# Kernel optimization log

Measured on AMD Instinct MI355X. Metric: run time of the kernel, lower is better.

Reference implementation:

```python
import jax, jax.numpy as jnp
import numpy as np

B, S, D = 2, 2048, 2048
H, KV, HD = 32, 8, 64          # n_heads, n_kv_heads, head_dim
REP = H // KV                  # 4
THETA = 10000.0


def _rotate_half(u):
    h = u.shape[-1] // 2
    return jnp.concatenate([-u[..., h:], u[..., :h]], axis=-1)


def setup_inputs() -> dict:
    key = jax.random.key(0)
    ks = jax.random.split(key, 5)
    x = jax.random.normal(ks[0], (B, S, D), dtype=jnp.float32)
    Wq = jax.random.normal(ks[1], (D, H * HD), dtype=jnp.float32) * 0.02
    Wk = jax.random.normal(ks[2], (D, KV * HD), dtype=jnp.float32) * 0.02
    Wv = jax.random.normal(ks[3], (D, KV * HD), dtype=jnp.float32) * 0.02
    Wo = jax.random.normal(ks[4], (H * HD, D), dtype=jnp.float32) * 0.02
    return {"x": x, "Wq": Wq, "Wk": Wk, "Wv": Wv, "Wo": Wo}


def reference(x, Wq, Wk, Wv, Wo):
    b, s, d = x.shape
    # QKV projections (nn.Linear, no bias)
    q = (x @ Wq).reshape(b, s, H, HD).transpose(0, 2, 1, 3)   # [B,H,S,HD]
    k = (x @ Wk).reshape(b, s, KV, HD).transpose(0, 2, 1, 3)  # [B,KV,S,HD]
    v = (x @ Wv).reshape(b, s, KV, HD).transpose(0, 2, 1, 3)  # [B,KV,S,HD]

    # RoPE (position_offset = 0)
    inv_freq = 1.0 / (THETA ** (jnp.arange(0, HD, 2, dtype=jnp.float32) / HD))
    freqs = jnp.outer(jnp.arange(s, dtype=jnp.float32), inv_freq)  # [S,HD/2]
    emb = jnp.concatenate([freqs, freqs], axis=-1)                  # [S,HD]
    cos, sin = jnp.cos(emb), jnp.sin(emb)
    q = q * cos + _rotate_half(q) * sin
    k = k * cos + _rotate_half(k) * sin

    # Grouped attention: avoid materializing repeated KV tensors.
    qg = q.reshape(b, KV, REP, s, HD)                               # [B,KV,REP,S,HD]
    scale = 1.0 / np.sqrt(HD)
    scores = jnp.einsum('bgrqd,bgkd->bgrqk', qg, k) * scale         # [B,KV,REP,S,S]
    causal = jnp.tril(jnp.ones((s, s), dtype=bool))
    scores = jnp.where(causal, scores, jnp.finfo(jnp.float32).min)
    probs = jax.nn.softmax(scores.astype(jnp.float32), axis=-1).astype(q.dtype)
    out = jnp.einsum('bgrqk,bgkd->bgrqd', probs, v)                 # [B,KV,REP,S,HD]
    out = out.reshape(b, H, s, HD).transpose(0, 2, 1, 3).reshape(b, s, H * HD)
    return out @ Wo                                                  # [B,S,D]
```

## Files before the change

kernel.cpp:

```cpp
#include <hip/hip_runtime.h>
#include <math.h>

typedef __bf16 bf16_t;
typedef bf16_t bf16x8 __attribute__((ext_vector_type(8)));
typedef bf16_t bf16x4 __attribute__((ext_vector_type(4)));
typedef float floatx4 __attribute__((ext_vector_type(4)));
typedef short short4v __attribute__((ext_vector_type(4)));

#define MFMA16(a, b, c) __builtin_amdgcn_mfma_f32_16x16x32_bf16((a), (b), (c), 0, 0, 0)

#if __has_builtin(__builtin_amdgcn_exp2f)
#define PEXP(x) __builtin_amdgcn_exp2f(x)
#define SCORE_SCALE (0.125f * 1.4426950408889634f)
#else
#define PEXP(x) __expf(x)
#define SCORE_SCALE 0.125f
#endif

#if __has_builtin(__builtin_amdgcn_mfma_f32_16x16x16bf16_1k)
#define HAVE_MFMA_K16 1
__device__ __forceinline__ floatx4 mfma_k16(bf16x4 a, bf16x4 b, floatx4 c)
{
    union { bf16x4 v; short4v s; } ua, ub;
    ua.v = a; ub.v = b;
    return __builtin_amdgcn_mfma_f32_16x16x16bf16_1k(ua.s, ub.s, c, 0, 0, 0);
}
#endif

union PU { unsigned u[2]; bf16x4 v; };
union BU { unsigned u[4]; bf16x8 v; };

__device__ __forceinline__ void gld16(const void* g, void* lds)
{
    __builtin_amdgcn_global_load_lds(
        reinterpret_cast<const __attribute__((address_space(1))) void*>(
            reinterpret_cast<uintptr_t>(g)),
        reinterpret_cast<__attribute__((address_space(3))) void*>(
            (unsigned int)reinterpret_cast<uintptr_t>(lds)),
        16, 0, 0);
}

template <int ROUNDS>
__device__ __forceinline__ void stage512(
    const bf16_t* __restrict__ g, int K, int row0, int k0,
    bf16_t* lds, int tid, int wave)
{
    #pragma unroll
    for (int i = 0; i < ROUNDS; ++i) {
        int c = i * 512 + tid;
        int r = c >> 3, s = c & 7;
        gld16(g + (size_t)(row0 + r) * K + k0 + ((s ^ (r & 7)) << 3),
              lds + (size_t)(i * 512 + wave * 64) * 8);
    }
}

template <typename TC, int BN>
__device__ __forceinline__ void gemm256_body(
    const bf16_t* __restrict__ A, const bf16_t* __restrict__ Bt,
    TC* __restrict__ C, int row0, int col0, int N, int K, bf16_t* smem)
{
    constexpr int NT = BN / 64;
    constexpr int RB = BN / 64;
    constexpr int LPT = 4 + RB;

    const int tid  = threadIdx.x;
    const int wave = tid >> 6, lane = tid & 63;
    const int quad = lane >> 4, l16 = lane & 15;
    const int wm = (wave >> 2) * 128;
    const int wn = (wave & 3) * (BN / 4);

    bf16_t* As0 = smem;
    bf16_t* As1 = smem + 256 * 64;
    bf16_t* Bs0 = smem + 2 * 256 * 64;
    bf16_t* Bs1 = Bs0 + BN * 64;

    floatx4 acc[8][NT] = {};

    const int ntile = K >> 6;

    stage512<4>(A, K, row0, 0, As0, tid, wave);
    stage512<RB>(Bt, K, col0, 0, Bs0, tid, wave);

    #pragma unroll 1
    for (int t = 0; t < ntile; ++t) {
        const int cur = t & 1;
        bf16_t* Asc = cur ? As1 : As0;
        bf16_t* Bsc = cur ? Bs1 : Bs0;
        bf16_t* Asn = cur ? As0 : As1;
        bf16_t* Bsn = cur ? Bs0 : Bs1;

        if (t + 1 < ntile) {
            stage512<4>(A, K, row0, (t + 1) << 6, Asn, tid, wave);
            stage512<RB>(Bt, K, col0, (t + 1) << 6, Bsn, tid, wave);
            if constexpr (LPT == 8)
                __asm__ volatile("s_waitcnt vmcnt(8)" ::: "memory");
            else
                __asm__ volatile("s_waitcnt vmcnt(6)" ::: "memory");
        } else {
            __asm__ volatile("s_waitcnt vmcnt(0)" ::: "memory");
        }
        __builtin_amdgcn_s_barrier();
        __asm__ volatile("" ::: "memory");

        #pragma unroll
        for (int kh = 0; kh < 2; ++kh) {
            bf16x8 af[8], bfr[NT];
            #pragma unroll
            for (int mt = 0; mt < 8; ++mt) {
                int ar = wm + mt * 16 + l16;
                af[mt] = *(const bf16x8*)&Asc[ar * 64 + (((kh * 4 + quad) ^ (ar & 7)) << 3)];
            }
            #pragma unroll
            for (int nt = 0; nt < NT; ++nt) {
                int br = wn + nt * 16 + l16;
                bfr[nt] = *(const bf16x8*)&Bsc[br * 64 + (((kh * 4 + quad) ^ (br & 7)) << 3)];
            }
            __builtin_amdgcn_s_setprio(1);
            #pragma unroll
            for (int mt = 0; mt < 8; ++mt)
                #pragma unroll
                for (int nt = 0; nt < NT; ++nt)
                    acc[mt][nt] = MFMA16(af[mt], bfr[nt], acc[mt][nt]);
            __builtin_amdgcn_s_setprio(0);
        }
        __asm__ volatile("s_waitcnt lgkmcnt(0)" ::: "memory");
        __builtin_amdgcn_s_barrier();
    }

    #pragma unroll
    for (int mt = 0; mt < 8; ++mt)
        #pragma unroll
        for (int nt = 0; nt < NT; ++nt)
            #pragma unroll
            for (int r = 0; r < 4; ++r)
                C[(size_t)(row0 + wm + mt * 16 + quad * 4 + r) * N
                  + col0 + wn + nt * 16 + l16] = (TC)acc[mt][nt][r];
}

__global__ __launch_bounds__(512, 2) void gemm256_qkv(
    const bf16_t* __restrict__ A, const bf16_t* __restrict__ BtQ,
    const bf16_t* __restrict__ BtK, const bf16_t* __restrict__ BtV,
    bf16_t* __restrict__ CQ, bf16_t* __restrict__ CK, bf16_t* __restrict__ CV)
{
    extern __shared__ __align__(16) bf16_t smem[];
    const int x = blockIdx.x;
    const bf16_t* Bt; bf16_t* C; int N, col0;
    if (x < 8)       { Bt = BtQ; C = CQ; N = 2048; col0 = x * 256; }
    else if (x < 10) { Bt = BtK; C = CK; N = 512;  col0 = (x - 8) * 256; }
    else             { Bt = BtV; C = CV; N = 512;  col0 = (x - 10) * 256; }
    gemm256_body<bf16_t, 256>(A, Bt, C, blockIdx.y * 256, col0, N, 2048, smem);
}

__global__ __launch_bounds__(512, 2) void gemm256_out(
    const bf16_t* __restrict__ A, const bf16_t* __restrict__ Bt,
    float* __restrict__ C)
{
    extern __shared__ __align__(16) bf16_t smem[];
    gemm256_body<float, 128>(A, Bt, C, blockIdx.y * 256, blockIdx.x * 128,
                             2048, 2048, smem);
}

__device__ __forceinline__ void transpose_body(
    const float* __restrict__ W, bf16_t* __restrict__ Wt, int K, int N,
    int bx, int by, float (*t)[33], int tid)
{
    int tx = tid & 31, ty = tid >> 5;
    #pragma unroll
    for (int i = 0; i < 32; i += 8)
        t[ty + i][tx] = W[(size_t)(by + ty + i) * N + bx + tx];
    __syncthreads();
    #pragma unroll
    for (int i = 0; i < 32; i += 8)
        Wt[(size_t)(bx + ty + i) * K + by + tx] = (bf16_t)t[tx][ty + i];
}

__global__ __launch_bounds__(256) void prep_all(
    const float* __restrict__ x, const float* __restrict__ Wq,
    const float* __restrict__ Wk, const float* __restrict__ Wv,
    bf16_t* __restrict__ xb, bf16_t* __restrict__ WqT,
    bf16_t* __restrict__ WkT, bf16_t* __restrict__ WvT)
{
    __shared__ float t[32][33];
    const int blk = blockIdx.x, tid = threadIdx.x;
    if (blk < 8192) {
        int i = blk * 256 + tid;
        float4 f = ((const float4*)x)[i];
        bf16x4 v = {(bf16_t)f.x, (bf16_t)f.y, (bf16_t)f.z, (bf16_t)f.w};
        ((bf16x4*)xb)[i] = v;
    } else if (blk < 12288) {
        int r = blk - 8192;
        transpose_body(Wq, WqT, 2048, 2048, (r & 63) * 32, (r >> 6) * 32, t, tid);
    } else if (blk < 13312) {
        int r = blk - 12288;
        transpose_body(Wk, WkT, 2048, 512, (r & 15) * 32, (r >> 4) * 32, t, tid);
    } else {
        int r = blk - 13312;
        transpose_body(Wv, WvT, 2048, 512, (r & 15) * 32, (r >> 4) * 32, t, tid);
    }
}

__global__ __launch_bounds__(256) void mid_all(
    bf16_t* __restrict__ Kw, const bf16_t* __restrict__ Vw,
    bf16_t* __restrict__ VtG, const float* __restrict__ Wo,
    bf16_t* __restrict__ WoT)
{
    __shared__ float tf[32][33];
    __shared__ bf16_t tb[32][34];
    const int blk = blockIdx.x, tid = threadIdx.x;
    if (blk < 4096) {
        int idx = blk * 256 + tid;
        int i   = idx & 31;
        int h   = (idx >> 5) & 7;
        int row = idx >> 8;
        int pos = row & 2047;
        float invf = powf(10000.0f, -(float)i / 32.0f);
        float sv, cv;
        sincosf((float)pos * invf, &sv, &cv);
        size_t base = (size_t)row * 512 + (size_t)h * 64 + i;
        float a  = (float)Kw[base];
        float b2 = (float)Kw[base + 32];
        Kw[base]      = (bf16_t)(a * cv - b2 * sv);
        Kw[base + 32] = (bf16_t)(b2 * cv + a * sv);
    } else if (blk < 6144) {
        int r  = blk - 4096;
        int bz = r >> 10, r2 = r & 1023;
        int bx = (r2 & 15) * 32, by = (r2 >> 4) * 32;
        int tx = tid & 31, ty = tid >> 5;
        #pragma unroll
        for (int i = 0; i < 32; i += 8)
            tb[ty + i][tx] = Vw[((size_t)bz * 2048 + by + ty + i) * 512 + bx + tx];
        __syncthreads();
        #pragma unroll
        for (int i = 0; i < 32; i += 8)
            VtG[((size_t)bz * 512 + bx + ty + i) * 2048 + by + tx] = tb[tx][ty + i];
    } else {
        int r = blk - 6144;
        transpose_body(Wo, WoT, 2048, 2048, (r & 63) * 32, (r >> 6) * 32, tf, tid);
    }
}

__global__ __launch_bounds__(256) void gqa_attn(
    const bf16_t* __restrict__ Q, const bf16_t* __restrict__ Kc,
    const bf16_t* __restrict__ Vt, bf16_t* __restrict__ AO)
{
    __shared__ alignas(16) bf16_t Ks[2][64 * 64];
    __shared__ alignas(16) bf16_t Vs[2][64 * 64];

    const int x = blockIdx.x, h = blockIdx.y, b = blockIdx.z, g = h >> 2;
    const int tid  = threadIdx.x;
    const int wave = tid >> 6, lane = tid & 63;
    const int quad = lane >> 4, l16 = lane & 15;

    #pragma unroll 1
    for (int t = 0; t < 2; ++t) {
        const int qt = t ? x : (15 - x);
        const int q0 = qt * 128;
        int qb[2];
        qb[0] = q0 + wave * 16;
        qb[1] = qb[0] + 64;

        bf16x8 qf[2][2];
        #pragma unroll
        for (int mt = 0; mt < 2; ++mt) {
            int qrow = qb[mt] + l16;
            const bf16_t* qp = Q + (size_t)(b * 2048 + qrow) * 2048 + h * 64 + quad * 8;
            bf16x8 lo = *(const bf16x8*)qp;
            bf16x8 hi = *(const bf16x8*)(qp + 32);
            #pragma unroll
            for (int j = 0; j < 8; ++j) {
                int d = quad * 8 + j;
                float invf = powf(10000.0f, -(float)d / 32.0f);
                float sv, cv;
                sincosf((float)qrow * invf, &sv, &cv);
                float a = (float)lo[j], c2 = (float)hi[j];
                qf[mt][0][j] = (bf16_t)((a * cv - c2 * sv) * SCORE_SCALE);
                qf[mt][1][j] = (bf16_t)((c2 * cv + a * sv) * SCORE_SCALE);
            }
        }

        floatx4 o[2][4] = {};
        floatx4 ls4[2] = {};

        const int ktmax = 2 * qt + 1;

        __asm__ volatile("s_waitcnt lgkmcnt(0)" ::: "memory");
        __builtin_amdgcn_s_barrier();
        #pragma unroll
        for (int i = 0; i < 2; ++i) {
            int c = i * 256 + tid;
            int r = c >> 3, s = c & 7;
            int sw = (s ^ (r & 7)) << 3;
            gld16(Kc + (size_t)(b * 2048 + r) * 512 + g * 64 + sw,
                  &Ks[0][(i * 256 + wave * 64) * 8]);
            gld16(Vt + (size_t)(b * 512 + g * 64 + r) * 2048 + sw,
                  &Vs[0][(i * 256 + wave * 64) * 8]);
        }

        #pragma unroll 1
        for (int kt = 0; kt <= ktmax; ++kt) {
            const int cur = kt & 1;
            if (kt < ktmax) {
                const int kn = kt + 1;
                #pragma unroll
                for (int i = 0; i < 2; ++i) {
                    int c = i * 256 + tid;
                    int r = c >> 3, s = c & 7;
                    int sw = (s ^ (r & 7)) << 3;
                    gld16(Kc + (size_t)(b * 2048 + kn * 64 + r) * 512 + g * 64 + sw,
                          &Ks[cur ^ 1][(i * 256 + wave * 64) * 8]);
                    gld16(Vt + (size_t)(b * 512 + g * 64 + r) * 2048 + kn * 64 + sw,
                          &Vs[cur ^ 1][(i * 256 + wave * 64) * 8]);
                }
                __asm__ volatile("s_waitcnt vmcnt(4)" ::: "memory");
            } else {
                __asm__ volatile("s_waitcnt vmcnt(0)" ::: "memory");
            }
            __builtin_amdgcn_s_barrier();

            bool en[2];
            en[0] = (kt * 64) <= (qb[0] + 15);
            en[1] = (kt * 64) <= (qb[1] + 15);

            floatx4 st[2][4] = {};
            #pragma unroll
            for (int nt = 0; nt < 4; ++nt) {
                int kr = nt * 16 + l16;
                bf16x8 kf0 = *(const bf16x8*)&Ks[cur][kr * 64 + ((quad ^ (kr & 7)) << 3)];
                bf16x8 kf1 = *(const bf16x8*)&Ks[cur][kr * 64 + (((4 + quad) ^ (kr & 7)) << 3)];
                if (en[0]) {
                    st[0][nt] = MFMA16(kf0, qf[0][0], st[0][nt]);
                    st[0][nt] = MFMA16(kf1, qf[0][1], st[0][nt]);
                }
                if (en[1]) {
                    st[1][nt] = MFMA16(kf0, qf[1][0], st[1][nt]);
                    st[1][nt] = MFMA16(kf1, qf[1][1], st[1][nt]);
                }
            }

            PU pk[2][4];
            #pragma unroll
            for (int mt = 0; mt < 2; ++mt) {
                if (!en[mt]) continue;
                const bool diag = (kt * 64 + 63) > qb[mt];
                const int qa = qb[mt] + l16;
                #pragma unroll
                for (int nt = 0; nt < 4; ++nt) {
                    float pv[4];
                    #pragma unroll
                    for (int r = 0; r < 4; ++r) {
                        float e = PEXP(st[mt][nt][r]);
                        if (diag) {
                            int ka = kt * 64 + nt * 16 + quad * 4 + r;
                            if (ka > qa) e = 0.f;
                        }
                        ls4[mt][r] += e;
                        pv[r] = e;
                    }
                    pk[mt][nt].v = bf16x4{(bf16_t)pv[0], (bf16_t)pv[1],
                                          (bf16_t)pv[2], (bf16_t)pv[3]};
                }
            }

#ifdef HAVE_MFMA_K16
            #pragma unroll
            for (int nt = 0; nt < 4; ++nt)
                #pragma unroll
                for (int dt = 0; dt < 4; ++dt) {
                    int vr = dt * 16 + l16;
                    int slot = ((nt << 1) | (quad >> 1)) ^ (vr & 7);
                    bf16x4 va = *(const bf16x4*)&Vs[cur][vr * 64 + (slot << 3)
                                                         + ((quad & 1) << 2)];
                    if (en[0]) o[0][dt] = mfma_k16(va, pk[0][nt].v, o[0][dt]);
                    if (en[1]) o[1][dt] = mfma_k16(va, pk[1][nt].v, o[1][dt]);
                }
#else
            #pragma unroll
            for (int H = 0; H < 2; ++H) {
                BU bfv[2];
                #pragma unroll
                for (int mt = 0; mt < 2; ++mt) {
                    if (!en[mt]) continue;
                    #pragma unroll
                    for (int j = 0; j < 4; ++j) {
                        int srcl = (((quad & 1) << 1) + (j >> 1)) * 16 + l16;
                        unsigned a0 = (unsigned)__shfl((int)pk[mt][2 * H].u[j & 1], srcl, 64);
                        unsigned a1 = (unsigned)__shfl((int)pk[mt][2 * H + 1].u[j & 1], srcl, 64);
                        bfv[mt].u[j] = (quad >> 1) ? a1 : a0;
                    }
                }
                #pragma unroll
                for (int dt = 0; dt < 4; ++dt) {
                    int vr = dt * 16 + l16;
                    bf16x8 va = *(const bf16x8*)&Vs[cur][vr * 64
                                  + ((((H << 2) | quad) ^ (vr & 7)) << 3)];
                    if (en[0]) o[0][dt] = MFMA16(va, bfv[0].v, o[0][dt]);
                    if (en[1]) o[1][dt] = MFMA16(va, bfv[1].v, o[1][dt]);
                }
            }
#endif
            __asm__ volatile("s_waitcnt lgkmcnt(0)" ::: "memory");
            __builtin_amdgcn_s_barrier();
        }

        #pragma unroll
        for (int mt = 0; mt < 2; ++mt) {
            float l = ls4[mt][0] + ls4[mt][1] + ls4[mt][2] + ls4[mt][3];
            l += __shfl_xor(l, 16, 64);
            l += __shfl_xor(l, 32, 64);
            float rc = 1.0f / l;
            #pragma unroll
            for (int dt = 0; dt < 4; ++dt) {
                bf16x4 ov = {(bf16_t)(o[mt][dt][0] * rc), (bf16_t)(o[mt][dt][1] * rc),
                             (bf16_t)(o[mt][dt][2] * rc), (bf16_t)(o[mt][dt][3] * rc)};
                *(bf16x4*)&AO[(size_t)(b * 2048 + qb[mt] + l16) * 2048
                              + h * 64 + dt * 16 + quad * 4] = ov;
            }
        }
    }
}

extern "C" void kernel_launch(void* const* d_in, const int* in_sizes, int n_in,
                              void* d_out, int out_size, void* d_ws, size_t ws_size,
                              hipStream_t stream)
{
    const float* x  = (const float*)d_in[0];
    const float* Wq = (const float*)d_in[1];
    const float* Wk = (const float*)d_in[2];
    const float* Wv = (const float*)d_in[3];
    const float* Wo = (const float*)d_in[4];
    float* out = (float*)d_out;

    const size_t MB = 1024 * 1024;
    char* ws = (char*)d_ws;
    bf16_t* xb_AO = (bf16_t*)(ws);
    bf16_t* WqoT  = (bf16_t*)(ws + 16 * MB);
    bf16_t* WkT   = (bf16_t*)(ws + 24 * MB);
    bf16_t* WvT   = (bf16_t*)(ws + 26 * MB);
    bf16_t* Qw    = (bf16_t*)(ws + 28 * MB);
    bf16_t* Kw    = (bf16_t*)(ws + 44 * MB);
    bf16_t* Vw    = (bf16_t*)(ws + 48 * MB);
    bf16_t* VtG   = (bf16_t*)(ws + 52 * MB);

    static bool s_attr = false;
    if (!s_attr) {
        hipFuncSetAttribute(reinterpret_cast<const void*>(gemm256_qkv),
                            hipFuncAttributeMaxDynamicSharedMemorySize, 131072);
        hipFuncSetAttribute(reinterpret_cast<const void*>(gemm256_out),
                            hipFuncAttributeMaxDynamicSharedMemorySize, 98304);
        s_attr = true;
    }

    prep_all<<<14336, 256, 0, stream>>>(x, Wq, Wk, Wv, xb_AO, WqoT, WkT, WvT);

    gemm256_qkv<<<dim3(12, 16), 512, 131072, stream>>>(
        xb_AO, WqoT, WkT, WvT, Qw, Kw, Vw);

    mid_all<<<10240, 256, 0, stream>>>(Kw, Vw, VtG, Wo, WqoT);

    gqa_attn<<<dim3(8, 32, 2), 256, 0, stream>>>(Qw, Kw, VtG, xb_AO);

    gemm256_out<<<dim3(16, 16), 512, 98304, stream>>>(xb_AO, WqoT, out);
}
```

Before: 312.7 us.

## Use 8-phase interleaved GEMM pipeline and one q-tile per attention block

```diff
diff --git a/kernel.cpp b/kernel.cpp
--- a/kernel.cpp
+++ b/kernel.cpp
@@ -40,91 +40,119 @@
         16, 0, 0);
 }
 
-template <int ROUNDS>
-__device__ __forceinline__ void stage512(
-    const bf16_t* __restrict__ g, int K, int row0, int k0,
-    bf16_t* lds, int tid, int wave)
-{
-    #pragma unroll
-    for (int i = 0; i < ROUNDS; ++i) {
-        int c = i * 512 + tid;
-        int r = c >> 3, s = c & 7;
-        gld16(g + (size_t)(row0 + r) * K + k0 + ((s ^ (r & 7)) << 3),
-              lds + (size_t)(i * 512 + wave * 64) * 8);
-    }
-}
+#define STAGE_A(dst, h, u) do {                                               \
+    bf16_t* _b = (dst) ? As1 : As0;                                           \
+    _Pragma("unroll")                                                         \
+    for (int _i = 0; _i < 2; ++_i) {                                          \
+        int _c = _i * 512 + tid, _r = _c >> 3, _s = _c & 7;                   \
+        gld16(A + (size_t)(row0 + (h) * 128 + _r) * K + ((u) << 6)            \
+                + ((_s ^ (_r & 7)) << 3),                                     \
+              _b + (h) * 8192 + (_i * 512 + wave * 64) * 8);                  \
+    } } while (0)
+
+#define STAGE_B(dst, h, u) do {                                               \
+    bf16_t* _b = (dst) ? Bs1 : Bs0;                                           \
+    _Pragma("unroll")                                                         \
+    for (int _i = 0; _i < RB_; ++_i) {                                        \
+        int _c = _i * 512 + tid, _r = _c >> 3, _s = _c & 7;                   \
+        gld16(Bt + (size_t)(col0 + (h) * (BN / 2) + _r) * K + ((u) << 6)      \
+                 + ((_s ^ (_r & 7)) << 3),                                    \
+              _b + (h) * (BN / 2) * 64 + (_i * 512 + wave * 64) * 8);         \
+    } } while (0)
+
+#define PHASE(MTB, NTB, READA, READB) do {                                    \
+    if (READA) {                                                              \
+        _Pragma("unroll")                                                     \
+        for (int _i = 0; _i < 4; ++_i)                                        \
+            _Pragma("unroll")                                                 \
+            for (int _kh = 0; _kh < 2; ++_kh) {                               \
+                int _ar = wm + ((MTB) + _i) * 16 + l16;                       \
+                af[_i][_kh] = *(const bf16x8*)&Asd[_ar * 64 +                 \
+                    (((_kh * 4 + quad) ^ (_ar & 7)) << 3)];                   \
+            }                                                                 \
+    }                                                                         \
+    if (READB) {                                                              \
+        _Pragma("unroll")                                                     \
+        for (int _j = 0; _j < NTH; ++_j)                                      \
+            _Pragma("unroll")                                                 \
+            for (int _kh = 0; _kh < 2; ++_kh) {                               \
+                int _br = wn + ((NTB) + _j) * 16 + l16;                       \
+                bfr[_j][_kh] = *(const bf16x8*)&Bsd[_br * 64 +                \
+                    (((_kh * 4 + quad) ^ (_br & 7)) << 3)];                   \
+            }                                                                 \
+    }                                                                         \
+    __asm__ volatile("s_waitcnt lgkmcnt(0)" ::: "memory");                    \
+    __builtin_amdgcn_sched_barrier(0);                                        \
+    __builtin_amdgcn_s_setprio(1);                                            \
+    _Pragma("unroll")                                                         \
+    for (int _kh = 0; _kh < 2; ++_kh)                                         \
+        _Pragma("unroll")                                                     \
+        for (int _i = 0; _i < 4; ++_i)                                        \
+            _Pragma("unroll")                                                 \
+            for (int _j = 0; _j < NTH; ++_j)                                  \
+                acc[(MTB) + _i][(NTB) + _j] =                                 \
+                    MFMA16(af[_i][_kh], bfr[_j][_kh],                         \
+                           acc[(MTB) + _i][(NTB) + _j]);                      \
+    __builtin_amdgcn_s_setprio(0);                                            \
+    __builtin_amdgcn_s_barrier();                                             \
+    __builtin_amdgcn_sched_barrier(0);                                        \
+} while (0)
 
 template <typename TC, int BN>
-__device__ __forceinline__ void gemm256_body(
+__device__ __forceinline__ void gemm8p_body(
     const bf16_t* __restrict__ A, const bf16_t* __restrict__ Bt,
     TC* __restrict__ C, int row0, int col0, int N, int K, bf16_t* smem)
 {
-    constexpr int NT = BN / 64;
-    constexpr int RB = BN / 64;
-    constexpr int LPT = 4 + RB;
+    constexpr int WN  = BN / 4;
+    constexpr int NT  = WN / 16;
+    constexpr int NTH = NT / 2;
+    constexpr int RB_ = BN / 128;
 
     const int tid  = threadIdx.x;
     const int wave = tid >> 6, lane = tid & 63;
     const int quad = lane >> 4, l16 = lane & 15;
     const int wm = (wave >> 2) * 128;
-    const int wn = (wave & 3) * (BN / 4);
+    const int wn = (wave & 3) * WN;
 
     bf16_t* As0 = smem;
     bf16_t* As1 = smem + 256 * 64;
     bf16_t* Bs0 = smem + 2 * 256 * 64;
     bf16_t* Bs1 = Bs0 + BN * 64;
 
+    const int ntile = K >> 6;
+
     floatx4 acc[8][NT] = {};
-
-    const int ntile = K >> 6;
-
-    stage512<4>(A, K, row0, 0, As0, tid, wave);
-    stage512<RB>(Bt, K, col0, 0, Bs0, tid, wave);
+    bf16x8  af[4][2];
+    bf16x8  bfr[NTH][2];
+
+    STAGE_A(0, 0, 0); STAGE_A(0, 1, 0);
+    STAGE_B(0, 0, 0); STAGE_B(0, 1, 0);
+    STAGE_A(1, 0, 1);
 
     #pragma unroll 1
-    for (int t = 0; t < ntile; ++t) {
-        const int cur = t & 1;
-        bf16_t* Asc = cur ? As1 : As0;
-        bf16_t* Bsc = cur ? Bs1 : Bs0;
-        bf16_t* Asn = cur ? As0 : As1;
-        bf16_t* Bsn = cur ? Bs0 : Bs1;
-
-        if (t + 1 < ntile) {
-            stage512<4>(A, K, row0, (t + 1) << 6, Asn, tid, wave);
-            stage512<RB>(Bt, K, col0, (t + 1) << 6, Bsn, tid, wave);
-            if constexpr (LPT == 8)
-                __asm__ volatile("s_waitcnt vmcnt(8)" ::: "memory");
-            else
-                __asm__ volatile("s_waitcnt vmcnt(6)" ::: "memory");
+    for (int u = 0; u < ntile; ++u) {
+        const int d = u & 1;
+        bf16_t* Asd = d ? As1 : As0;
+        bf16_t* Bsd = d ? Bs1 : Bs0;
+
+        if (u + 1 < ntile) {
+            STAGE_A(d ^ 1, 1, u + 1);
+            __asm__ volatile("s_waitcnt vmcnt(4)" ::: "memory");
         } else {
             __asm__ volatile("s_waitcnt vmcnt(0)" ::: "memory");
         }
         __builtin_amdgcn_s_barrier();
-        __asm__ volatile("" ::: "memory");
-
-        #pragma unroll
-        for (int kh = 0; kh < 2; ++kh) {
-            bf16x8 af[8], bfr[NT];
-            #pragma unroll
-            for (int mt = 0; mt < 8; ++mt) {
-                int ar = wm + mt * 16 + l16;
-                af[mt] = *(const bf16x8*)&Asc[ar * 64 + (((kh * 4 + quad) ^ (ar & 7)) << 3)];
-            }
-            #pragma unroll
-            for (int nt = 0; nt < NT; ++nt) {
-                int br = wn + nt * 16 + l16;
-                bfr[nt] = *(const bf16x8*)&Bsc[br * 64 + (((kh * 4 + quad) ^ (br & 7)) << 3)];
-            }
-            __builtin_amdgcn_s_setprio(1);
-            #pragma unroll
-            for (int mt = 0; mt < 8; ++mt)
-                #pragma unroll
-                for (int nt = 0; nt < NT; ++nt)
-                    acc[mt][nt] = MFMA16(af[mt], bfr[nt], acc[mt][nt]);
-            __builtin_amdgcn_s_setprio(0);
-        }
-        __asm__ volatile("s_waitcnt lgkmcnt(0)" ::: "memory");
-        __builtin_amdgcn_s_barrier();
+        __builtin_amdgcn_sched_barrier(0);
+        PHASE(0, 0, true, true);
+
+        if (u + 1 < ntile) STAGE_B(d ^ 1, 0, u + 1);
+        PHASE(0, NTH, false, true);
+
+        if (u + 1 < ntile) STAGE_B(d ^ 1, 1, u + 1);
+        PHASE(4, NTH, true, false);
+
+        if (u + 2 < ntile) STAGE_A(d, 0, u + 2);
+        PHASE(4, 0, false, true);
     }
 
     #pragma unroll
@@ -137,7 +165,7 @@
                   + col0 + wn + nt * 16 + l16] = (TC)acc[mt][nt][r];
 }
 
-__global__ __launch_bounds__(512, 2) void gemm256_qkv(
+__global__ __launch_bounds__(512, 2) void gemm8p_qkv(
     const bf16_t* __restrict__ A, const bf16_t* __restrict__ BtQ,
     const bf16_t* __restrict__ BtK, const bf16_t* __restrict__ BtV,
     bf16_t* __restrict__ CQ, bf16_t* __restrict__ CK, bf16_t* __restrict__ CV)
@@ -148,16 +176,16 @@
     if (x < 8)       { Bt = BtQ; C = CQ; N = 2048; col0 = x * 256; }
     else if (x < 10) { Bt = BtK; C = CK; N = 512;  col0 = (x - 8) * 256; }
     else             { Bt = BtV; C = CV; N = 512;  col0 = (x - 10) * 256; }
-    gemm256_body<bf16_t, 256>(A, Bt, C, blockIdx.y * 256, col0, N, 2048, smem);
-}
-
-__global__ __launch_bounds__(512, 2) void gemm256_out(
+    gemm8p_body<bf16_t, 256>(A, Bt, C, blockIdx.y * 256, col0, N, 2048, smem);
+}
+
+__global__ __launch_bounds__(512, 2) void gemm8p_out(
     const bf16_t* __restrict__ A, const bf16_t* __restrict__ Bt,
     float* __restrict__ C)
 {
     extern __shared__ __align__(16) bf16_t smem[];
-    gemm256_body<float, 128>(A, Bt, C, blockIdx.y * 256, blockIdx.x * 128,
-                             2048, 2048, smem);
+    gemm8p_body<float, 128>(A, Bt, C, blockIdx.y * 256, blockIdx.x * 128,
+                            2048, 2048, smem);
 }
 
 __device__ __forceinline__ void transpose_body(
@@ -246,175 +274,169 @@
     __shared__ alignas(16) bf16_t Ks[2][64 * 64];
     __shared__ alignas(16) bf16_t Vs[2][64 * 64];
 
-    const int x = blockIdx.x, h = blockIdx.y, b = blockIdx.z, g = h >> 2;
+    const int qt = blockIdx.x, h = blockIdx.y, b = blockIdx.z, g = h >> 2;
     const int tid  = threadIdx.x;
     const int wave = tid >> 6, lane = tid & 63;
     const int quad = lane >> 4, l16 = lane & 15;
 
+    const int q0 = qt * 128;
+    int qb[2];
+    qb[0] = q0 + wave * 16;
+    qb[1] = qb[0] + 64;
+
+    bf16x8 qf[2][2];
+    #pragma unroll
+    for (int mt = 0; mt < 2; ++mt) {
+        int qrow = qb[mt] + l16;
+        const bf16_t* qp = Q + (size_t)(b * 2048 + qrow) * 2048 + h * 64 + quad * 8;
+        bf16x8 lo = *(const bf16x8*)qp;
+        bf16x8 hi = *(const bf16x8*)(qp + 32);
+        #pragma unroll
+        for (int j = 0; j < 8; ++j) {
+            int d = quad * 8 + j;
+            float invf = powf(10000.0f, -(float)d / 32.0f);
+            float sv, cv;
+            sincosf((float)qrow * invf, &sv, &cv);
+            float a = (float)lo[j], c2 = (float)hi[j];
+            qf[mt][0][j] = (bf16_t)((a * cv - c2 * sv) * SCORE_SCALE);
+            qf[mt][1][j] = (bf16_t)((c2 * cv + a * sv) * SCORE_SCALE);
+        }
+    }
+
+    floatx4 o[2][4] = {};
+    floatx4 ls4[2] = {};
+
+    const int ktmax = 2 * qt + 1;
+
+    #pragma unroll
+    for (int i = 0; i < 2; ++i) {
+        int c = i * 256 + tid;
+        int r = c >> 3, s = c & 7;
+        int sw = (s ^ (r & 7)) << 3;
+        gld16(Kc + (size_t)(b * 2048 + r) * 512 + g * 64 + sw,
+              &Ks[0][(i * 256 + wave * 64) * 8]);
+        gld16(Vt + (size_t)(b * 512 + g * 64 + r) * 2048 + sw,
+              &Vs[0][(i * 256 + wave * 64) * 8]);
+    }
+
     #pragma unroll 1
-    for (int t = 0; t < 2; ++t) {
-        const int qt = t ? x : (15 - x);
-        const int q0 = qt * 128;
-        int qb[2];
-        qb[0] = q0 + wave * 16;
-        qb[1] = qb[0] + 64;
-
-        bf16x8 qf[2][2];
+    for (int kt = 0; kt <= ktmax; ++kt) {
+        const int cur = kt & 1;
+        if (kt < ktmax) {
+            const int kn = kt + 1;
+            #pragma unroll
+            for (int i = 0; i < 2; ++i) {
+                int c = i * 256 + tid;
+                int r = c >> 3, s = c & 7;
+                int sw = (s ^ (r & 7)) << 3;
+                gld16(Kc + (size_t)(b * 2048 + kn * 64 + r) * 512 + g * 64 + sw,
+                      &Ks[cur ^ 1][(i * 256 + wave * 64) * 8]);
+                gld16(Vt + (size_t)(b * 512 + g * 64 + r) * 2048 + kn * 64 + sw,
+                      &Vs[cur ^ 1][(i * 256 + wave * 64) * 8]);
+            }
+            __asm__ volatile("s_waitcnt vmcnt(4)" ::: "memory");
+        } else {
+            __asm__ volatile("s_waitcnt vmcnt(0)" ::: "memory");
+        }
+        __builtin_amdgcn_s_barrier();
+
+        bool en[2];
+        en[0] = (kt * 64) <= (qb[0] + 15);
+        en[1] = (kt * 64) <= (qb[1] + 15);
+
+        floatx4 st[2][4] = {};
+        #pragma unroll
+        for (int nt = 0; nt < 4; ++nt) {
+            int kr = nt * 16 + l16;
+            bf16x8 kf0 = *(const bf16x8*)&Ks[cur][kr * 64 + ((quad ^ (kr & 7)) << 3)];
+            bf16x8 kf1 = *(const bf16x8*)&Ks[cur][kr * 64 + (((4 + quad) ^ (kr & 7)) << 3)];
+            if (en[0]) {
+                st[0][nt] = MFMA16(kf0, qf[0][0], st[0][nt]);
+                st[0][nt] = MFMA16(kf1, qf[0][1], st[0][nt]);
+            }
+            if (en[1]) {
+                st[1][nt] = MFMA16(kf0, qf[1][0], st[1][nt]);
+                st[1][nt] = MFMA16(kf1, qf[1][1], st[1][nt]);
+            }
+        }
+
+        PU pk[2][4];
         #pragma unroll
         for (int mt = 0; mt < 2; ++mt) {
-            int qrow = qb[mt] + l16;
-            const bf16_t* qp = Q + (size_t)(b * 2048 + qrow) * 2048 + h * 64 + quad * 8;
-            bf16x8 lo = *(const bf16x8*)qp;
-            bf16x8 hi = *(const bf16x8*)(qp + 32);
-            #pragma unroll
-            for (int j = 0; j < 8; ++j) {
-                int d = quad * 8 + j;
-                float invf = powf(10000.0f, -(float)d / 32.0f);
-                float sv, cv;
-                sincosf((float)qrow * invf, &sv, &cv);
-                float a = (float)lo[j], c2 = (float)hi[j];
-                qf[mt][0][j] = (bf16_t)((a * cv - c2 * sv) * SCORE_SCALE);
-                qf[mt][1][j] = (bf16_t)((c2 * cv + a * sv) * SCORE_SCALE);
-            }
-        }
-
-        floatx4 o[2][4] = {};
-        floatx4 ls4[2] = {};
-
-        const int ktmax = 2 * qt + 1;
-
+            if (!en[mt]) continue;
+            const bool diag = (kt * 64 + 63) > qb[mt];
+            const int qa = qb[mt] + l16;
+            #pragma unroll
+            for (int nt = 0; nt < 4; ++nt) {
+                float pv[4];
+                #pragma unroll
+                for (int r = 0; r < 4; ++r) {
+                    float e = PEXP(st[mt][nt][r]);
+                    if (diag) {
+                        int ka = kt * 64 + nt * 16 + quad * 4 + r;
+                        if (ka > qa) e = 0.f;
+                    }
+                    ls4[mt][r] += e;
+                    pv[r] = e;
+                }
+                pk[mt][nt].v = bf16x4{(bf16_t)pv[0], (bf16_t)pv[1],
+                                      (bf16_t)pv[2], (bf16_t)pv[3]};
+            }
+        }
+
+#ifdef HAVE_MFMA_K16
+        #pragma unroll
+        for (int nt = 0; nt < 4; ++nt)
+            #pragma unroll
+            for (int dt = 0; dt < 4; ++dt) {
+                int vr = dt * 16 + l16;
+                int slot = ((nt << 1) | (quad >> 1)) ^ (vr & 7);
+                bf16x4 va = *(const bf16x4*)&Vs[cur][vr * 64 + (slot << 3)
+                                                     + ((quad & 1) << 2)];
+                if (en[0]) o[0][dt] = mfma_k16(va, pk[0][nt].v, o[0][dt]);
+                if (en[1]) o[1][dt] = mfma_k16(va, pk[1][nt].v, o[1][dt]);
+            }
+#else
+        #pragma unroll
+        for (int H = 0; H < 2; ++H) {
+            BU bfv[2];
+            #pragma unroll
+            for (int mt = 0; mt < 2; ++mt) {
+                if (!en[mt]) continue;
+                #pragma unroll
+                for (int j = 0; j < 4; ++j) {
+                    int srcl = (((quad & 1) << 1) + (j >> 1)) * 16 + l16;
+                    unsigned a0 = (unsigned)__shfl((int)pk[mt][2 * H].u[j & 1], srcl, 64);
+                    unsigned a1 = (unsigned)__shfl((int)pk[mt][2 * H + 1].u[j & 1], srcl, 64);
+                    bfv[mt].u[j] = (quad >> 1) ? a1 : a0;
+                }
+            }
+            #pragma unroll
+            for (int dt = 0; dt < 4; ++dt) {
+                int vr = dt * 16 + l16;
+                bf16x8 va = *(const bf16x8*)&Vs[cur][vr * 64
+                              + ((((H << 2) | quad) ^ (vr & 7)) << 3)];
+                if (en[0]) o[0][dt] = MFMA16(va, bfv[0].v, o[0][dt]);
+                if (en[1]) o[1][dt] = MFMA16(va, bfv[1].v, o[1][dt]);
+            }
+        }
+#endif
         __asm__ volatile("s_waitcnt lgkmcnt(0)" ::: "memory");
         __builtin_amdgcn_s_barrier();
-        #pragma unroll
-        for (int i = 0; i < 2; ++i) {
-            int c = i * 256 + tid;
-            int r = c >> 3, s = c & 7;
-            int sw = (s ^ (r & 7)) << 3;
-            gld16(Kc + (size_t)(b * 2048 + r) * 512 + g * 64 + sw,
-                  &Ks[0][(i * 256 + wave * 64) * 8]);
-            gld16(Vt + (size_t)(b * 512 + g * 64 + r) * 2048 + sw,
-                  &Vs[0][(i * 256 + wave * 64) * 8]);
-        }
-
-        #pragma unroll 1
-        for (int kt = 0; kt <= ktmax; ++kt) {
-            const int cur = kt & 1;
-            if (kt < ktmax) {
-                const int kn = kt + 1;
-                #pragma unroll
-                for (int i = 0; i < 2; ++i) {
-                    int c = i * 256 + tid;
-                    int r = c >> 3, s = c & 7;
-                    int sw = (s ^ (r & 7)) << 3;
-                    gld16(Kc + (size_t)(b * 2048 + kn * 64 + r) * 512 + g * 64 + sw,
-                          &Ks[cur ^ 1][(i * 256 + wave * 64) * 8]);
-                    gld16(Vt + (size_t)(b * 512 + g * 64 + r) * 2048 + kn * 64 + sw,
-                          &Vs[cur ^ 1][(i * 256 + wave * 64) * 8]);
-                }
-                __asm__ volatile("s_waitcnt vmcnt(4)" ::: "memory");
-            } else {
-                __asm__ volatile("s_waitcnt vmcnt(0)" ::: "memory");
-            }
-            __builtin_amdgcn_s_barrier();
-
-            bool en[2];
-            en[0] = (kt * 64) <= (qb[0] + 15);
-            en[1] = (kt * 64) <= (qb[1] + 15);
-
-            floatx4 st[2][4] = {};
-            #pragma unroll
-            for (int nt = 0; nt < 4; ++nt) {
-                int kr = nt * 16 + l16;
-                bf16x8 kf0 = *(const bf16x8*)&Ks[cur][kr * 64 + ((quad ^ (kr & 7)) << 3)];
-                bf16x8 kf1 = *(const bf16x8*)&Ks[cur][kr * 64 + (((4 + quad) ^ (kr & 7)) << 3)];
-                if (en[0]) {
-                    st[0][nt] = MFMA16(kf0, qf[0][0], st[0][nt]);
-                    st[0][nt] = MFMA16(kf1, qf[0][1], st[0][nt]);
-                }
-                if (en[1]) {
-                    st[1][nt] = MFMA16(kf0, qf[1][0], st[1][nt]);
-                    st[1][nt] = MFMA16(kf1, qf[1][1], st[1][nt]);
-                }
-            }
-
-            PU pk[2][4];
-            #pragma unroll
-            for (int mt = 0; mt < 2; ++mt) {
-                if (!en[mt]) continue;
-                const bool diag = (kt * 64 + 63) > qb[mt];
-                const int qa = qb[mt] + l16;
-                #pragma unroll
-                for (int nt = 0; nt < 4; ++nt) {
-                    float pv[4];
-                    #pragma unroll
-                    for (int r = 0; r < 4; ++r) {
-                        float e = PEXP(st[mt][nt][r]);
-                        if (diag) {
-                            int ka = kt * 64 + nt * 16 + quad * 4 + r;
-                            if (ka > qa) e = 0.f;
-                        }
-                        ls4[mt][r] += e;
-                        pv[r] = e;
-                    }
-                    pk[mt][nt].v = bf16x4{(bf16_t)pv[0], (bf16_t)pv[1],
-                                          (bf16_t)pv[2], (bf16_t)pv[3]};
-                }
-            }
-
-#ifdef HAVE_MFMA_K16
-            #pragma unroll
-            for (int nt = 0; nt < 4; ++nt)
-                #pragma unroll
-                for (int dt = 0; dt < 4; ++dt) {
-                    int vr = dt * 16 + l16;
-                    int slot = ((nt << 1) | (quad >> 1)) ^ (vr & 7);
-                    bf16x4 va = *(const bf16x4*)&Vs[cur][vr * 64 + (slot << 3)
-                                                         + ((quad & 1) << 2)];
-                    if (en[0]) o[0][dt] = mfma_k16(va, pk[0][nt].v, o[0][dt]);
-                    if (en[1]) o[1][dt] = mfma_k16(va, pk[1][nt].v, o[1][dt]);
-                }
-#else
-            #pragma unroll
-            for (int H = 0; H < 2; ++H) {
-                BU bfv[2];
-                #pragma unroll
-                for (int mt = 0; mt < 2; ++mt) {
-                    if (!en[mt]) continue;
-                    #pragma unroll
-                    for (int j = 0; j < 4; ++j) {
-                        int srcl = (((quad & 1) << 1) + (j >> 1)) * 16 + l16;
-                        unsigned a0 = (unsigned)__shfl((int)pk[mt][2 * H].u[j & 1], srcl, 64);
-                        unsigned a1 = (unsigned)__shfl((int)pk[mt][2 * H + 1].u[j & 1], srcl, 64);
-                        bfv[mt].u[j] = (quad >> 1) ? a1 : a0;
-                    }
-                }
-                #pragma unroll
-                for (int dt = 0; dt < 4; ++dt) {
-                    int vr = dt * 16 + l16;
-                    bf16x8 va = *(const bf16x8*)&Vs[cur][vr * 64
-                                  + ((((H << 2) | quad) ^ (vr & 7)) << 3)];
-                    if (en[0]) o[0][dt] = MFMA16(va, bfv[0].v, o[0][dt]);
-                    if (en[1]) o[1][dt] = MFMA16(va, bfv[1].v, o[1][dt]);
-                }
-            }
-#endif
-            __asm__ volatile("s_waitcnt lgkmcnt(0)" ::: "memory");
-            __builtin_amdgcn_s_barrier();
-        }
-
-        #pragma unroll
-        for (int mt = 0; mt < 2; ++mt) {
-            float l = ls4[mt][0] + ls4[mt][1] + ls4[mt][2] + ls4[mt][3];
-            l += __shfl_xor(l, 16, 64);
-            l += __shfl_xor(l, 32, 64);
-            float rc = 1.0f / l;
-            #pragma unroll
-            for (int dt = 0; dt < 4; ++dt) {
-                bf16x4 ov = {(bf16_t)(o[mt][dt][0] * rc), (bf16_t)(o[mt][dt][1] * rc),
-                             (bf16_t)(o[mt][dt][2] * rc), (bf16_t)(o[mt][dt][3] * rc)};
-                *(bf16x4*)&AO[(size_t)(b * 2048 + qb[mt] + l16) * 2048
-                              + h * 64 + dt * 16 + quad * 4] = ov;
-            }
+    }
+
+    #pragma unroll
+    for (int mt = 0; mt < 2; ++mt) {
+        float l = ls4[mt][0] + ls4[mt][1] + ls4[mt][2] + ls4[mt][3];
+        l += __shfl_xor(l, 16, 64);
+        l += __shfl_xor(l, 32, 64);
+        float rc = 1.0f / l;
+        #pragma unroll
+        for (int dt = 0; dt < 4; ++dt) {
+            bf16x4 ov = {(bf16_t)(o[mt][dt][0] * rc), (bf16_t)(o[mt][dt][1] * rc),
+                         (bf16_t)(o[mt][dt][2] * rc), (bf16_t)(o[mt][dt][3] * rc)};
+            *(bf16x4*)&AO[(size_t)(b * 2048 + qb[mt] + l16) * 2048
+                          + h * 64 + dt * 16 + quad * 4] = ov;
         }
     }
 }
@@ -443,21 +465,21 @@
 
     static bool s_attr = false;
     if (!s_attr) {
-        hipFuncSetAttribute(reinterpret_cast<const void*>(gemm256_qkv),
+        hipFuncSetAttribute(reinterpret_cast<const void*>(gemm8p_qkv),
                             hipFuncAttributeMaxDynamicSharedMemorySize, 131072);
-        hipFuncSetAttribute(reinterpret_cast<const void*>(gemm256_out),
+        hipFuncSetAttribute(reinterpret_cast<const void*>(gemm8p_out),
                             hipFuncAttributeMaxDynamicSharedMemorySize, 98304);
         s_attr = true;
     }
 
     prep_all<<<14336, 256, 0, stream>>>(x, Wq, Wk, Wv, xb_AO, WqoT, WkT, WvT);
 
-    gemm256_qkv<<<dim3(12, 16), 512, 131072, stream>>>(
+    gemm8p_qkv<<<dim3(12, 16), 512, 131072, stream>>>(
         xb_AO, WqoT, WkT, WvT, Qw, Kw, Vw);
 
     mid_all<<<10240, 256, 0, stream>>>(Kw, Vw, VtG, Wo, WqoT);
 
-    gqa_attn<<<dim3(8, 32, 2), 256, 0, stream>>>(Qw, Kw, VtG, xb_AO);
-
-    gemm256_out<<<dim3(16, 16), 512, 98304, stream>>>(xb_AO, WqoT, out);
-}
+    gqa_attn<<<dim3(16, 32, 2), 256, 0, stream>>>(Qw, Kw, VtG, xb_AO);
+
+    gemm8p_out<<<dim3(16, 16), 512, 98304, stream>>>(xb_AO, WqoT, out);
+}
```

New measurement: 374.0 us. 1.2x slower.
